# Kernel tuning notes

Hardware: AMD Instinct MI355X
Metric: run time of the kernel (lower is better)

The kernel has to match this reference:

```python
import jax, jax.numpy as jnp
import numpy as np

NUM_GRAPHS = 64  # number of graphs in the batch for global_mean_pool
BN_EPS = 1e-5


def setup_inputs() -> dict:
    key = jax.random.key(0)
    ks = jax.random.split(key, 8)
    N, E, D, H, O = 100000, 1600000, 128, 128, 32
    x = jax.random.normal(ks[0], (N, D), dtype=jnp.float32)
    edge_index = jax.random.randint(ks[1], (2, E), 0, N, dtype=jnp.int64)
    batch = jnp.sort(jax.random.randint(ks[2], (N,), 0, NUM_GRAPHS, dtype=jnp.int64))
    s = 1.0 / np.sqrt(D)
    W0 = (jax.random.normal(ks[3], (D, H), dtype=jnp.float32) * s)
    b0 = jnp.zeros((H,), jnp.float32)
    g0 = jnp.ones((H,), jnp.float32)
    be0 = jnp.zeros((H,), jnp.float32)
    W1 = (jax.random.normal(ks[4], (H, H), dtype=jnp.float32) * s)
    b1 = jnp.zeros((H,), jnp.float32)
    g1 = jnp.ones((H,), jnp.float32)
    be1 = jnp.zeros((H,), jnp.float32)
    Wfc = (jax.random.normal(ks[5], (H, O), dtype=jnp.float32) * s)
    bfc = jnp.zeros((O,), jnp.float32)
    return dict(x=x, edge_index=edge_index, batch=batch,
                W0=W0, b0=b0, g0=g0, be0=be0,
                W1=W1, b1=b1, g1=g1, be1=be1,
                Wfc=Wfc, bfc=bfc)


def reference(x, edge_index, batch, W0, b0, g0, be0, W1, b1, g1, be1, Wfc, bfc):
    N = x.shape[0]
    loops = jnp.arange(N, dtype=edge_index.dtype)
    src = jnp.concatenate([edge_index[0], loops])  # [E+N]
    dst = jnp.concatenate([edge_index[1], loops])
    # GCN symmetric normalization on A + I
    deg = jax.ops.segment_sum(jnp.ones_like(dst, jnp.float32), dst, num_segments=N)
    dinv = jnp.where(deg > 0, jax.lax.rsqrt(deg), 0.0)
    norm = dinv[src] * dinv[dst]  # [E+N]

    def gcn_layer(h, W, b):
        h = h @ W                                   # [N, H] transform first (PyG GCNConv)
        msg = h[src] * norm[:, None]                # gather + scale
        agg = jax.ops.segment_sum(msg, dst, num_segments=N)  # scatter-add
        return agg + b

    def bn_relu(h, g, be):  # BatchNorm1d (batch stats, biased var) + ReLU
        mu = h.mean(axis=0)
        var = h.var(axis=0)
        return jax.nn.relu((h - mu) * jax.lax.rsqrt(var + BN_EPS) * g + be)

    h = bn_relu(gcn_layer(x, W0, b0), g0, be0)
    h = bn_relu(gcn_layer(h, W1, b1), g1, be1)

    # global_mean_pool over graph assignment
    cnt = jax.ops.segment_sum(jnp.ones((N,), jnp.float32), batch, num_segments=NUM_GRAPHS)
    pooled = jax.ops.segment_sum(h, batch, num_segments=NUM_GRAPHS)
    pooled = pooled / jnp.maximum(cnt, 1.0)[:, None]
    return pooled @ Wfc + bfc  # [NUM_GRAPHS, out_dim]
```

## Files before the change

### kernel.cpp

```cpp
#include <hip/hip_runtime.h>

typedef short bf16x8 __attribute__((ext_vector_type(8)));
typedef float f32x4 __attribute__((ext_vector_type(4)));

#define NBLK 512
#define NSTAT 512

__device__ __forceinline__ unsigned short f2bf(float f) {
    unsigned u = __float_as_uint(f);
    u += 0x7fffu + ((u >> 16) & 1u);
    return (unsigned short)(u >> 16);
}
__device__ __forceinline__ float bflo(unsigned u) { return __uint_as_float(u << 16); }
__device__ __forceinline__ float bfhi(unsigned u) { return __uint_as_float(u & 0xffff0000u); }


__global__ __launch_bounds__(256) void kb_count(const int* __restrict__ dst, int E, int nb,
                                                int chunk, int* __restrict__ counts) {
    __shared__ int h[512];
    for (int i = threadIdx.x; i < 512; i += 256) h[i] = 0;
    __syncthreads();
    int e0 = blockIdx.x * chunk, e1 = min(e0 + chunk, E);
    for (int e = e0 + threadIdx.x; e < e1; e += 256) atomicAdd(&h[dst[e] >> 8], 1);
    __syncthreads();
    for (int b = threadIdx.x; b < nb; b += 256) counts[b * NBLK + blockIdx.x] = h[b];
}

__global__ __launch_bounds__(NBLK) void kb_offsets(int* __restrict__ counts,
                                                   int* __restrict__ total) {
    __shared__ int s[NBLK];
    int b = blockIdx.x, t = threadIdx.x;
    int v = counts[b * NBLK + t];
    s[t] = v; __syncthreads();
    for (int off = 1; off < NBLK; off <<= 1) {
        int x = (t >= off) ? s[t - off] : 0;
        __syncthreads();
        s[t] += x;
        __syncthreads();
    }
    counts[b * NBLK + t] = s[t] - v;
    if (t == NBLK - 1) total[b] = s[t];
}

__global__ __launch_bounds__(512) void kb_base(const int* __restrict__ total, int nb,
                                               int* __restrict__ bbase) {
    __shared__ int s[512];
    int t = threadIdx.x;
    int v = (t < nb) ? total[t] : 0;
    s[t] = v; __syncthreads();
    for (int off = 1; off < 512; off <<= 1) {
        int x = (t >= off) ? s[t - off] : 0;
        __syncthreads();
        s[t] += x;
        __syncthreads();
    }
    if (t < nb) bbase[t] = s[t] - v;
}

__global__ __launch_bounds__(NBLK) void kb_scatter(const int* __restrict__ src,
                                                   const int* __restrict__ dst, int E, int nb,
                                                   int chunk,
                                                   const int* __restrict__ counts,
                                                   const int* __restrict__ bbase,
                                                   int2* __restrict__ rec) {
    __shared__ int cur[512];
    int t = threadIdx.x;
    if (t < nb) cur[t] = bbase[t] + counts[t * NBLK + blockIdx.x];
    __syncthreads();
    int e0 = blockIdx.x * chunk, e1 = min(e0 + chunk, E);
    for (int e = e0 + t; e < e1; e += NBLK) {
        int s = src[e], d = dst[e];
        int pos = atomicAdd(&cur[d >> 8], 1);
        rec[pos] = make_int2(s, d);
    }
}

__global__ __launch_bounds__(256) void kb_deg(const int2* __restrict__ rec,
                                              const int* __restrict__ bbase,
                                              const int* __restrict__ total,
                                              int* __restrict__ deg,
                                              float* __restrict__ dinv, int N) {
    __shared__ int dc[256];
    int b = blockIdx.x, t = threadIdx.x;
    dc[t] = 0; __syncthreads();
    int r0 = bbase[b], r1 = r0 + total[b];
    for (int i = r0 + t; i < r1; i += 256) atomicAdd(&dc[rec[i].y & 255], 1);
    __syncthreads();
    int gn = b * 256 + t;
    if (gn < N) {
        int d = dc[t];
        deg[gn] = d;
        dinv[gn] = rsqrtf((float)(d + 1));
    }
}

__global__ __launch_bounds__(256) void k_scan_part(const int* __restrict__ deg, int N,
                                                   int* __restrict__ part) {
    int base = blockIdx.x * 1024 + threadIdx.x * 4;
    int s = 0;
#pragma unroll
    for (int i = 0; i < 4; ++i) {
        int idx = base + i;
        if (idx < N) s += (deg[idx] + 7) & ~7;
    }
    __shared__ int red[256];
    red[threadIdx.x] = s; __syncthreads();
    for (int off = 128; off > 0; off >>= 1) {
        if (threadIdx.x < off) red[threadIdx.x] += red[threadIdx.x + off];
        __syncthreads();
    }
    if (threadIdx.x == 0) part[blockIdx.x] = red[0];
}
__global__ void k_scan_mid(int* part, int nb) {
    if (threadIdx.x == 0 && blockIdx.x == 0) {
        int run = 0;
        for (int i = 0; i < nb; ++i) { int t = part[i]; part[i] = run; run += t; }
    }
}
__global__ __launch_bounds__(256) void k_scan_final(const int* __restrict__ deg, int N,
                                                    const int* __restrict__ part,
                                                    int* __restrict__ rowptr) {
    int t = threadIdx.x;
    int base = blockIdx.x * 1024 + t * 4;
    int v[4]; int s = 0;
#pragma unroll
    for (int i = 0; i < 4; ++i) {
        int idx = base + i;
        v[i] = (idx < N) ? ((deg[idx] + 7) & ~7) : 0;
        s += v[i];
    }
    __shared__ int sc[256];
    sc[t] = s; __syncthreads();
    for (int off = 1; off < 256; off <<= 1) {
        int x = (t >= off) ? sc[t - off] : 0;
        __syncthreads();
        sc[t] += x;
        __syncthreads();
    }
    int excl = sc[t] - s + part[blockIdx.x];
#pragma unroll
    for (int i = 0; i < 4; ++i) {
        int idx = base + i;
        if (idx < N) { rowptr[idx] = excl; excl += v[i]; }
    }
}

__global__ __launch_bounds__(256) void kb_place(const int2* __restrict__ rec,
                                                const int* __restrict__ bbase,
                                                const int* __restrict__ total,
                                                const int* __restrict__ rowptr,
                                                const float* __restrict__ dinv,
                                                int2* __restrict__ csr, int N) {
    __shared__ int cur[256];
    int b = blockIdx.x, t = threadIdx.x;
    int gn = b * 256 + t;
    int rp = (gn < N) ? rowptr[gn] : 0;
    cur[t] = rp;
    __syncthreads();
    int r0 = bbase[b], r1 = r0 + total[b];
    for (int i = r0 + t; i < r1; i += 256) {
        int2 rc = rec[i];
        int pos = atomicAdd(&cur[rc.y & 255], 1);
        float w = dinv[rc.x] * dinv[rc.y];
        csr[pos] = make_int2(rc.x, __float_as_int(w));
    }
    __syncthreads();
    if (gn < N) {
        int end = cur[t];
        int pe = rp + ((end - rp + 7) & ~7);
        for (int i = end; i < pe; ++i) csr[i] = make_int2(0, 0);
    }
}

__global__ __launch_bounds__(256) void k_wprep(const float* __restrict__ W0,
                                               const float* __restrict__ W1,
                                               unsigned short* __restrict__ W0t,
                                               unsigned short* __restrict__ W1t) {
    int tt = blockIdx.x * 256 + threadIdx.x;
    const float* W = (tt < 2048) ? W0 : W1;
    unsigned short* Wt = (tt < 2048) ? W0t : W1t;
    int t = tt & 2047;
    int f = t >> 6, lane = t & 63;
    int kc = f >> 3, nt = f & 7;
    int kbase = kc * 32 + (lane >> 4) * 8;
    int n = nt * 16 + (lane & 15);
    unsigned short t8[8];
#pragma unroll
    for (int j = 0; j < 8; ++j) t8[j] = f2bf(W[(size_t)(kbase + j) * 128 + n]);
    unsigned short* o = &Wt[(size_t)t * 8];
    *(ushort4*)&o[0] = *(ushort4*)&t8[0];
    *(ushort4*)&o[4] = *(ushort4*)&t8[4];
}

__global__ __launch_bounds__(256) void k_gemm(const void* __restrict__ Xv,
                                              const unsigned short* __restrict__ Wt,
                                              const float* __restrict__ scale,
                                              const float* __restrict__ shift,
                                              unsigned short* __restrict__ Hout,
                                              int N, int xbf16) {
    __shared__ unsigned short sX[64 * 136];
    const int tid = threadIdx.x;
    const int rowBase = blockIdx.x * 64;

    if (!xbf16) {
        const float* X = (const float*)Xv;
#pragma unroll
        for (int i = 0; i < 8; ++i) {
            int f4 = tid + 256 * i;
            int r = f4 >> 5; int k4 = (f4 & 31) * 4;
            int gr = rowBase + r;
            float4 v = make_float4(0.f, 0.f, 0.f, 0.f);
            if (gr < N) v = *(const float4*)&X[(size_t)gr * 128 + k4];
            ushort4 p;
            p.x = f2bf(v.x); p.y = f2bf(v.y); p.z = f2bf(v.z); p.w = f2bf(v.w);
            *(ushort4*)&sX[r * 136 + k4] = p;
        }
    } else {
        const int4* X = (const int4*)Xv;
#pragma unroll
        for (int i = 0; i < 4; ++i) {
            int f8 = tid + 256 * i;
            int r = f8 >> 4; int k8 = (f8 & 15) * 8;
            int gr = rowBase + r;
            int4 u = make_int4(0, 0, 0, 0);
            if (gr < N) u = X[(size_t)gr * 16 + (f8 & 15)];
            float fv[8] = { bflo(u.x), bfhi(u.x), bflo(u.y), bfhi(u.y),
                            bflo(u.z), bfhi(u.z), bflo(u.w), bfhi(u.w) };
            unsigned short t8[8];
#pragma unroll
            for (int j = 0; j < 8; ++j)
                t8[j] = f2bf(fmaxf(fmaf(fv[j], scale[k8 + j], shift[k8 + j]), 0.f));
            *(ushort4*)&sX[r * 136 + k8]     = *(ushort4*)&t8[0];
            *(ushort4*)&sX[r * 136 + k8 + 4] = *(ushort4*)&t8[4];
        }
    }
    __syncthreads();

    const int lane = tid & 63, wave = tid >> 6;
    const int m = lane & 15, q = lane >> 4;
    const int rowOff = (wave * 16 + m) * 136 + q * 8;
    f32x4 acc[8];
#pragma unroll
    for (int nt = 0; nt < 8; ++nt) acc[nt] = (f32x4){0.f, 0.f, 0.f, 0.f};
    const bf16x8* WtF = (const bf16x8*)Wt;
#pragma unroll
    for (int kc = 0; kc < 4; ++kc) {
        bf16x8 xb = *(const bf16x8*)&sX[rowOff + kc * 32];
#pragma unroll
        for (int nt = 0; nt < 8; ++nt) {
            bf16x8 wa = WtF[(kc * 8 + nt) * 64 + lane];
            acc[nt] = __builtin_amdgcn_mfma_f32_16x16x32_bf16(wa, xb, acc[nt], 0, 0, 0);
        }
    }
    int grow = rowBase + wave * 16 + m;
    if (grow < N) {
#pragma unroll
        for (int nt = 0; nt < 8; ++nt) {
            ushort4 p;
            p.x = f2bf(acc[nt][0]); p.y = f2bf(acc[nt][1]);
            p.z = f2bf(acc[nt][2]); p.w = f2bf(acc[nt][3]);
            *(ushort4*)&Hout[(size_t)grow * 128 + nt * 16 + q * 4] = p;
        }
    }
}

__global__ __launch_bounds__(256) void k_agg(const unsigned short* __restrict__ H,
                                             const int* __restrict__ rowptr,
                                             const int* __restrict__ deg,
                                             const int2* __restrict__ csr,
                                             const float* __restrict__ dinv,
                                             const float* __restrict__ bias,
                                             unsigned* __restrict__ out, int N) {
    int wave = threadIdx.x >> 6;
    int lane = threadIdx.x & 63;
    int node = blockIdx.x * 4 + wave;
    if (node >= N) return;
    const unsigned* Hu = (const unsigned*)H;
    int start = rowptr[node];
    int pd = (deg[node] + 7) & ~7;
    float a0 = 0.f, a1 = 0.f;
    const int4* cp = (const int4*)(csr + start);
    int j = 0;
    for (; j + 16 <= pd; j += 16) {
        int4 q0 = cp[0], q1 = cp[1], q2 = cp[2], q3 = cp[3];
        int4 q4 = cp[4], q5 = cp[5], q6 = cp[6], q7 = cp[7];
        cp += 8;
        unsigned u0 = Hu[(size_t)q0.x * 64 + lane];
        unsigned u1 = Hu[(size_t)q0.z * 64 + lane];
        unsigned u2 = Hu[(size_t)q1.x * 64 + lane];
        unsigned u3 = Hu[(size_t)q1.z * 64 + lane];
        unsigned u4 = Hu[(size_t)q2.x * 64 + lane];
        unsigned u5 = Hu[(size_t)q2.z * 64 + lane];
        unsigned u6 = Hu[(size_t)q3.x * 64 + lane];
        unsigned u7 = Hu[(size_t)q3.z * 64 + lane];
        unsigned u8 = Hu[(size_t)q4.x * 64 + lane];
        unsigned u9 = Hu[(size_t)q4.z * 64 + lane];
        unsigned uA = Hu[(size_t)q5.x * 64 + lane];
        unsigned uB = Hu[(size_t)q5.z * 64 + lane];
        unsigned uC = Hu[(size_t)q6.x * 64 + lane];
        unsigned uD = Hu[(size_t)q6.z * 64 + lane];
        unsigned uE = Hu[(size_t)q7.x * 64 + lane];
        unsigned uF = Hu[(size_t)q7.z * 64 + lane];
        float w0 = __int_as_float(q0.y), w1 = __int_as_float(q0.w);
        float w2 = __int_as_float(q1.y), w3 = __int_as_float(q1.w);
        float w4 = __int_as_float(q2.y), w5 = __int_as_float(q2.w);
        float w6 = __int_as_float(q3.y), w7 = __int_as_float(q3.w);
        float w8 = __int_as_float(q4.y), w9 = __int_as_float(q4.w);
        float wA = __int_as_float(q5.y), wB = __int_as_float(q5.w);
        float wC = __int_as_float(q6.y), wD = __int_as_float(q6.w);
        float wE = __int_as_float(q7.y), wF = __int_as_float(q7.w);
        a0 = fmaf(w0, bflo(u0), a0); a1 = fmaf(w0, bfhi(u0), a1);
        a0 = fmaf(w1, bflo(u1), a0); a1 = fmaf(w1, bfhi(u1), a1);
        a0 = fmaf(w2, bflo(u2), a0); a1 = fmaf(w2, bfhi(u2), a1);
        a0 = fmaf(w3, bflo(u3), a0); a1 = fmaf(w3, bfhi(u3), a1);
        a0 = fmaf(w4, bflo(u4), a0); a1 = fmaf(w4, bfhi(u4), a1);
        a0 = fmaf(w5, bflo(u5), a0); a1 = fmaf(w5, bfhi(u5), a1);
        a0 = fmaf(w6, bflo(u6), a0); a1 = fmaf(w6, bfhi(u6), a1);
        a0 = fmaf(w7, bflo(u7), a0); a1 = fmaf(w7, bfhi(u7), a1);
        a0 = fmaf(w8, bflo(u8), a0); a1 = fmaf(w8, bfhi(u8), a1);
        a0 = fmaf(w9, bflo(u9), a0); a1 = fmaf(w9, bfhi(u9), a1);
        a0 = fmaf(wA, bflo(uA), a0); a1 = fmaf(wA, bfhi(uA), a1);
        a0 = fmaf(wB, bflo(uB), a0); a1 = fmaf(wB, bfhi(uB), a1);
        a0 = fmaf(wC, bflo(uC), a0); a1 = fmaf(wC, bfhi(uC), a1);
        a0 = fmaf(wD, bflo(uD), a0); a1 = fmaf(wD, bfhi(uD), a1);
        a0 = fmaf(wE, bflo(uE), a0); a1 = fmaf(wE, bfhi(uE), a1);
        a0 = fmaf(wF, bflo(uF), a0); a1 = fmaf(wF, bfhi(uF), a1);
    }
    if (j < pd) {
        int4 q0 = cp[0], q1 = cp[1], q2 = cp[2], q3 = cp[3];
        unsigned u0 = Hu[(size_t)q0.x * 64 + lane];
        unsigned u1 = Hu[(size_t)q0.z * 64 + lane];
        unsigned u2 = Hu[(size_t)q1.x * 64 + lane];
        unsigned u3 = Hu[(size_t)q1.z * 64 + lane];
        unsigned u4 = Hu[(size_t)q2.x * 64 + lane];
        unsigned u5 = Hu[(size_t)q2.z * 64 + lane];
        unsigned u6 = Hu[(size_t)q3.x * 64 + lane];
        unsigned u7 = Hu[(size_t)q3.z * 64 + lane];
        float w0 = __int_as_float(q0.y), w1 = __int_as_float(q0.w);
        float w2 = __int_as_float(q1.y), w3 = __int_as_float(q1.w);
        float w4 = __int_as_float(q2.y), w5 = __int_as_float(q2.w);
        float w6 = __int_as_float(q3.y), w7 = __int_as_float(q3.w);
        a0 = fmaf(w0, bflo(u0), a0); a1 = fmaf(w0, bfhi(u0), a1);
        a0 = fmaf(w1, bflo(u1), a0); a1 = fmaf(w1, bfhi(u1), a1);
        a0 = fmaf(w2, bflo(u2), a0); a1 = fmaf(w2, bfhi(u2), a1);
        a0 = fmaf(w3, bflo(u3), a0); a1 = fmaf(w3, bfhi(u3), a1);
        a0 = fmaf(w4, bflo(u4), a0); a1 = fmaf(w4, bfhi(u4), a1);
        a0 = fmaf(w5, bflo(u5), a0); a1 = fmaf(w5, bfhi(u5), a1);
        a0 = fmaf(w6, bflo(u6), a0); a1 = fmaf(w6, bfhi(u6), a1);
        a0 = fmaf(w7, bflo(u7), a0); a1 = fmaf(w7, bfhi(u7), a1);
    }
    {
        float dn = dinv[node];
        float w = dn * dn;
        unsigned u = Hu[(size_t)node * 64 + lane];
        a0 = fmaf(w, bflo(u), a0);
        a1 = fmaf(w, bfhi(u), a1);
    }
    float2 bv = ((const float2*)bias)[lane];
    a0 += bv.x; a1 += bv.y;
    out[(size_t)node * 64 + lane] = (unsigned)f2bf(a0) | ((unsigned)f2bf(a1) << 16);
}

__global__ __launch_bounds__(256) void k_stats(const int4* __restrict__ B4, int N,
                                               float* __restrict__ P1,
                                               float* __restrict__ P2) {
    int tid = threadIdx.x;
    int lane = tid & 63, wave = tid >> 6;
    int c = lane & 15;
    int rsub = lane >> 4;
    float s1[8] = {0.f,0.f,0.f,0.f,0.f,0.f,0.f,0.f};
    float s2[8] = {0.f,0.f,0.f,0.f,0.f,0.f,0.f,0.f};
    for (int r = blockIdx.x * 16 + wave * 4 + rsub; r < N; r += NSTAT * 16) {
        int4 u = B4[(size_t)r * 16 + c];
        float f[8] = { bflo(u.x), bfhi(u.x), bflo(u.y), bfhi(u.y),
                       bflo(u.z), bfhi(u.z), bflo(u.w), bfhi(u.w) };
#pragma unroll
        for (int j = 0; j < 8; ++j) { s1[j] += f[j]; s2[j] = fmaf(f[j], f[j], s2[j]); }
    }
#pragma unroll
    for (int j = 0; j < 8; ++j) {
        s1[j] += __shfl_xor(s1[j], 16, 64);
        s1[j] += __shfl_xor(s1[j], 32, 64);
        s2[j] += __shfl_xor(s2[j], 16, 64);
        s2[j] += __shfl_xor(s2[j], 32, 64);
    }
    __shared__ float ls1[4][128], ls2[4][128];
    if (rsub == 0) {
#pragma unroll
        for (int j = 0; j < 8; ++j) { ls1[wave][c * 8 + j] = s1[j]; ls2[wave][c * 8 + j] = s2[j]; }
    }
    __syncthreads();
    if (tid < 128) {
        P1[blockIdx.x * 128 + tid] = ls1[0][tid] + ls1[1][tid] + ls1[2][tid] + ls1[3][tid];
        P2[blockIdx.x * 128 + tid] = ls2[0][tid] + ls2[1][tid] + ls2[2][tid] + ls2[3][tid];
    }
}

__global__ __launch_bounds__(256) void k_bnfinal(const float* __restrict__ P1,
                          const float* __restrict__ P2,
                          const float* __restrict__ g, const float* __restrict__ be,
                          float* __restrict__ scale, float* __restrict__ shift,
                          float invN) {
    __shared__ float sm[256];
    int t = threadIdx.x;
    int c = t & 127;
    const float* P = (t < 128) ? P1 : P2;
    float s = 0.f;
    for (int b = 0; b < NSTAT; ++b) s += P[b * 128 + c];
    sm[t] = s;
    __syncthreads();
    if (t < 128) {
        float mu = sm[t] * invN;
        float var = sm[t + 128] * invN - mu * mu;
        float sc = g[t] * rsqrtf(var + 1e-5f);
        scale[t] = sc;
        shift[t] = fmaf(-mu, sc, be[t]);
    }
}

__global__ __launch_bounds__(256) void k_hist(const int* __restrict__ batch, int N,
                                              int* __restrict__ gcnt) {
    __shared__ int h[64];
    if (threadIdx.x < 64) h[threadIdx.x] = 0;
    __syncthreads();
    for (int i = blockIdx.x * 256 + threadIdx.x; i < N; i += gridDim.x * 256)
        atomicAdd(&h[batch[i]], 1);
    __syncthreads();
    if (threadIdx.x < 64 && h[threadIdx.x]) atomicAdd(&gcnt[threadIdx.x], h[threadIdx.x]);
}

__global__ __launch_bounds__(256) void k_pool(const int4* __restrict__ B4,
                                              const float* __restrict__ scale,
                                              const float* __restrict__ shift,
                                              const int* __restrict__ batch, int N,
                                              int rpb, float* __restrict__ pooled) {
    int tid = threadIdx.x;
    int c = tid & 15;
    int rh = tid >> 4;
    int r0 = blockIdx.x * rpb;
    int r1 = min(r0 + rpb, N);
    float sc[8], sh[8];
#pragma unroll
    for (int j = 0; j < 8; ++j) { sc[j] = scale[c * 8 + j]; sh[j] = shift[c * 8 + j]; }
    float acc[8] = {0.f,0.f,0.f,0.f,0.f,0.f,0.f,0.f};
    int cur = -1;
    for (int r = r0 + rh; r < r1; r += 16) {
        int g = batch[r];
        if (g != cur) {
            if (cur >= 0) {
#pragma unroll
                for (int j = 0; j < 8; ++j)
                    atomicAdd(&pooled[cur * 128 + c * 8 + j], acc[j]);
            }
#pragma unroll
            for (int j = 0; j < 8; ++j) acc[j] = 0.f;
            cur = g;
        }
        int4 u = B4[(size_t)r * 16 + c];
        float f[8] = { bflo(u.x), bfhi(u.x), bflo(u.y), bfhi(u.y),
                       bflo(u.z), bfhi(u.z), bflo(u.w), bfhi(u.w) };
#pragma unroll
        for (int j = 0; j < 8; ++j) acc[j] += fmaxf(fmaf(f[j], sc[j], sh[j]), 0.f);
    }
    if (cur >= 0) {
#pragma unroll
        for (int j = 0; j < 8; ++j)
            atomicAdd(&pooled[cur * 128 + c * 8 + j], acc[j]);
    }
}

__global__ __launch_bounds__(256) void k_fc(const float* __restrict__ pooled,
                                            const int* __restrict__ gcnt,
                                            const float* __restrict__ Wfc,
                                            const float* __restrict__ bfc,
                                            float* __restrict__ out) {
    int idx = blockIdx.x * 256 + threadIdx.x;
    if (idx >= 64 * 32) return;
    int g = idx >> 5, o = idx & 31;
    float inv = 1.f / fmaxf((float)gcnt[g], 1.f);
    float acc = bfc[o];
    for (int k = 0; k < 128; ++k)
        acc = fmaf(pooled[g * 128 + k] * inv, Wfc[k * 32 + o], acc);
    out[idx] = acc;
}

extern "C" void kernel_launch(void* const* d_in, const int* in_sizes, int n_in,
                              void* d_out, int out_size, void* d_ws, size_t ws_size,
                              hipStream_t stream) {
    const float* x    = (const float*)d_in[0];
    const int*  eidx  = (const int*)d_in[1];
    const int*  batch = (const int*)d_in[2];
    const float* W0 = (const float*)d_in[3];
    const float* b0 = (const float*)d_in[4];
    const float* g0 = (const float*)d_in[5];
    const float* be0 = (const float*)d_in[6];
    const float* W1 = (const float*)d_in[7];
    const float* b1 = (const float*)d_in[8];
    const float* g1 = (const float*)d_in[9];
    const float* be1 = (const float*)d_in[10];
    const float* Wfc = (const float*)d_in[11];
    const float* bfc = (const float*)d_in[12];
    float* out = (float*)d_out;

    const int N = in_sizes[0] / 128;
    const int E = in_sizes[1] / 2;
    const int* esrc = eidx;
    const int* edst = eidx + E;
    const int NB = (N + 255) >> 8;
    const size_t paddedE = (size_t)E + 7 * (size_t)N;

    char* base = (char*)d_ws;
    size_t off = 0;
    auto take = [&](size_t bytes) -> char* {
        char* p = base + off;
        off = (off + bytes + 255) & ~(size_t)255;
        return p;
    };
    unsigned short* hA = (unsigned short*)take((size_t)N * 128 * 2);
    int2* rec = (int2*)hA;
    unsigned* B = (unsigned*)take((size_t)N * 64 * 4);
    int2* csr   = (int2*)take(paddedE * 8);
    int* rowptr = (int*)take((size_t)N * 4);
    int* deg    = (int*)take((size_t)N * 4);
    float* dinv = (float*)take((size_t)N * 4);
    int* counts = (int*)take((size_t)512 * NBLK * 4);
    int* total  = (int*)take(512 * 4);
    int* bbase  = (int*)take(512 * 4);
    int* part   = (int*)take(1024 * 4);
    unsigned short* W0t = (unsigned short*)take(16384 * 2);
    unsigned short* W1t = (unsigned short*)take(16384 * 2);
    float* P1 = (float*)take((size_t)NSTAT * 128 * 4);
    float* P2 = (float*)take((size_t)NSTAT * 128 * 4);
    char* zeroB0 = base + off;
    float* pooled = (float*)take(64 * 128 * 4);
    int*   gcnt   = (int*)take(64 * 4);
    size_t zeroB_bytes = (size_t)((base + off) - zeroB0);
    float* scale1 = (float*)take(128 * 4);
    float* shift1 = (float*)take(128 * 4);
    float* scale2 = (float*)take(128 * 4);
    float* shift2 = (float*)take(128 * 4);
    (void)ws_size; (void)n_in; (void)out_size;

    hipMemsetAsync(zeroB0, 0, zeroB_bytes, stream);

    k_wprep<<<16, 256, 0, stream>>>(W0, W1, W0t, W1t);

    const int CH256 = (E + NBLK - 1) / NBLK;
    kb_count<<<NBLK, 256, 0, stream>>>(edst, E, NB, CH256, counts);
    kb_offsets<<<NB, NBLK, 0, stream>>>(counts, total);
    kb_base<<<1, 512, 0, stream>>>(total, NB, bbase);
    kb_scatter<<<NBLK, NBLK, 0, stream>>>(esrc, edst, E, NB, CH256, counts, bbase, rec);
    kb_deg<<<NB, 256, 0, stream>>>(rec, bbase, total, deg, dinv, N);
    const int nbScan = (N + 1023) / 1024;
    k_scan_part<<<nbScan, 256, 0, stream>>>(deg, N, part);
    k_scan_mid<<<1, 64, 0, stream>>>(part, nbScan);
    k_scan_final<<<nbScan, 256, 0, stream>>>(deg, N, part, rowptr);
    kb_place<<<NB, 256, 0, stream>>>(rec, bbase, total, rowptr, dinv, csr, N);

    const int gGemm = (N + 63) / 64;
    const int gAgg  = (N + 3) / 4;
    const float invN = 1.0f / (float)N;

    k_gemm<<<gGemm, 256, 0, stream>>>(x, W0t, scale1, shift1, hA, N, 0);
    k_agg<<<gAgg, 256, 0, stream>>>(hA, rowptr, deg, csr, dinv, b0, B, N);
    k_stats<<<NSTAT, 256, 0, stream>>>((const int4*)B, N, P1, P2);
    k_bnfinal<<<1, 256, 0, stream>>>(P1, P2, g0, be0, scale1, shift1, invN);

    k_gemm<<<gGemm, 256, 0, stream>>>(B, W1t, scale1, shift1, hA, N, 1);
    k_agg<<<gAgg, 256, 0, stream>>>(hA, rowptr, deg, csr, dinv, b1, B, N);
    k_stats<<<NSTAT, 256, 0, stream>>>((const int4*)B, N, P1, P2);
    k_bnfinal<<<1, 256, 0, stream>>>(P1, P2, g1, be1, scale2, shift2, invN);

    k_hist<<<256, 256, 0, stream>>>(batch, N, gcnt);
    const int rpb = (N + 511) / 512;
    k_pool<<<(N + rpb - 1) / rpb, 256, 0, stream>>>((const int4*)B, scale2, shift2, batch, N, rpb, pooled);
    k_fc<<<8, 256, 0, stream>>>(pooled, gcnt, Wfc, bfc, out);
}
```

Baseline: 452.0 us.

## Fuse BN stats into aggregation, fold row-pointer scan into degree/place kernels

```diff
diff --git a/kernel.cpp b/kernel.cpp
--- a/kernel.cpp
+++ b/kernel.cpp
@@ -4,7 +4,6 @@
 typedef float f32x4 __attribute__((ext_vector_type(4)));
 
 #define NBLK 512
-#define NSTAT 512
 
 __device__ __forceinline__ unsigned short f2bf(float f) {
     unsigned u = __float_as_uint(f);
@@ -42,11 +41,11 @@
     if (t == NBLK - 1) total[b] = s[t];
 }
 
-__global__ __launch_bounds__(512) void kb_base(const int* __restrict__ total, int nb,
-                                               int* __restrict__ bbase) {
+__global__ __launch_bounds__(512) void kb_base(const int* __restrict__ in, int nb,
+                                               int* __restrict__ outb) {
     __shared__ int s[512];
     int t = threadIdx.x;
-    int v = (t < nb) ? total[t] : 0;
+    int v = (t < nb) ? in[t] : 0;
     s[t] = v; __syncthreads();
     for (int off = 1; off < 512; off <<= 1) {
         int x = (t >= off) ? s[t - off] : 0;
@@ -54,7 +53,7 @@
         s[t] += x;
         __syncthreads();
     }
-    if (t < nb) bbase[t] = s[t] - v;
+    if (t < nb) outb[t] = s[t] - v;
 }
 
 __global__ __launch_bounds__(NBLK) void kb_scatter(const int* __restrict__ src,
@@ -79,7 +78,8 @@
                                               const int* __restrict__ bbase,
                                               const int* __restrict__ total,
                                               int* __restrict__ deg,
-                                              float* __restrict__ dinv, int N) {
+                                              float* __restrict__ dinv,
+                                              int* __restrict__ padsum, int N) {
     __shared__ int dc[256];
     int b = blockIdx.x, t = threadIdx.x;
     dc[t] = 0; __syncthreads();
@@ -87,74 +87,44 @@
     for (int i = r0 + t; i < r1; i += 256) atomicAdd(&dc[rec[i].y & 255], 1);
     __syncthreads();
     int gn = b * 256 + t;
+    int d = dc[t];
+    int pd = (gn < N) ? ((d + 7) & ~7) : 0;
     if (gn < N) {
-        int d = dc[t];
         deg[gn] = d;
         dinv[gn] = rsqrtf((float)(d + 1));
     }
-}
-
-__global__ __launch_bounds__(256) void k_scan_part(const int* __restrict__ deg, int N,
-                                                   int* __restrict__ part) {
-    int base = blockIdx.x * 1024 + threadIdx.x * 4;
-    int s = 0;
-#pragma unroll
-    for (int i = 0; i < 4; ++i) {
-        int idx = base + i;
-        if (idx < N) s += (deg[idx] + 7) & ~7;
-    }
-    __shared__ int red[256];
-    red[threadIdx.x] = s; __syncthreads();
+    __syncthreads();
+    dc[t] = pd; __syncthreads();
     for (int off = 128; off > 0; off >>= 1) {
-        if (threadIdx.x < off) red[threadIdx.x] += red[threadIdx.x + off];
-        __syncthreads();
-    }
-    if (threadIdx.x == 0) part[blockIdx.x] = red[0];
-}
-__global__ void k_scan_mid(int* part, int nb) {
-    if (threadIdx.x == 0 && blockIdx.x == 0) {
-        int run = 0;
-        for (int i = 0; i < nb; ++i) { int t = part[i]; part[i] = run; run += t; }
-    }
-}
-__global__ __launch_bounds__(256) void k_scan_final(const int* __restrict__ deg, int N,
-                                                    const int* __restrict__ part,
-                                                    int* __restrict__ rowptr) {
-    int t = threadIdx.x;
-    int base = blockIdx.x * 1024 + t * 4;
-    int v[4]; int s = 0;
-#pragma unroll
-    for (int i = 0; i < 4; ++i) {
-        int idx = base + i;
-        v[i] = (idx < N) ? ((deg[idx] + 7) & ~7) : 0;
-        s += v[i];
-    }
-    __shared__ int sc[256];
-    sc[t] = s; __syncthreads();
-    for (int off = 1; off < 256; off <<= 1) {
-        int x = (t >= off) ? sc[t - off] : 0;
-        __syncthreads();
-        sc[t] += x;
-        __syncthreads();
-    }
-    int excl = sc[t] - s + part[blockIdx.x];
-#pragma unroll
-    for (int i = 0; i < 4; ++i) {
-        int idx = base + i;
-        if (idx < N) { rowptr[idx] = excl; excl += v[i]; }
-    }
+        if (t < off) dc[t] += dc[t + off];
+        __syncthreads();
+    }
+    if (t == 0) padsum[b] = dc[0];
 }
 
 __global__ __launch_bounds__(256) void kb_place(const int2* __restrict__ rec,
                                                 const int* __restrict__ bbase,
                                                 const int* __restrict__ total,
-                                                const int* __restrict__ rowptr,
+                                                const int* __restrict__ bucketBase,
+                                                const int* __restrict__ deg,
                                                 const float* __restrict__ dinv,
-                                                int2* __restrict__ csr, int N) {
+                                                int2* __restrict__ csr,
+                                                int* __restrict__ rowptr, int N) {
+    __shared__ int sc[256];
     __shared__ int cur[256];
     int b = blockIdx.x, t = threadIdx.x;
     int gn = b * 256 + t;
-    int rp = (gn < N) ? rowptr[gn] : 0;
+    int d = (gn < N) ? deg[gn] : 0;
+    int pd = (d + 7) & ~7;
+    sc[t] = pd; __syncthreads();
+    for (int off = 1; off < 256; off <<= 1) {
+        int x = (t >= off) ? sc[t - off] : 0;
+        __syncthreads();
+        sc[t] += x;
+        __syncthreads();
+    }
+    int rp = bucketBase[b] + sc[t] - pd;
+    if (gn < N) rowptr[gn] = rp;
     cur[t] = rp;
     __syncthreads();
     int r0 = bbase[b], r1 = r0 + total[b];
@@ -167,7 +137,7 @@
     __syncthreads();
     if (gn < N) {
         int end = cur[t];
-        int pe = rp + ((end - rp + 7) & ~7);
+        int pe = rp + pd;
         for (int i = end; i < pe; ++i) csr[i] = make_int2(0, 0);
     }
 }
@@ -175,8 +145,13 @@
 __global__ __launch_bounds__(256) void k_wprep(const float* __restrict__ W0,
                                                const float* __restrict__ W1,
                                                unsigned short* __restrict__ W0t,
-                                               unsigned short* __restrict__ W1t) {
+                                               unsigned short* __restrict__ W1t,
+                                               float* __restrict__ pooled,
+                                               int* __restrict__ gcnt) {
     int tt = blockIdx.x * 256 + threadIdx.x;
+    pooled[tt] = 0.f;
+    pooled[tt + 4096] = 0.f;
+    if (tt < 64) gcnt[tt] = 0;
     const float* W = (tt < 2048) ? W0 : W1;
     unsigned short* Wt = (tt < 2048) ? W0t : W1t;
     int t = tt & 2047;
@@ -270,129 +245,114 @@
                                              const int2* __restrict__ csr,
                                              const float* __restrict__ dinv,
                                              const float* __restrict__ bias,
-                                             unsigned* __restrict__ out, int N) {
-    int wave = threadIdx.x >> 6;
-    int lane = threadIdx.x & 63;
-    int node = blockIdx.x * 4 + wave;
-    if (node >= N) return;
+                                             unsigned* __restrict__ out,
+                                             float* __restrict__ P1,
+                                             float* __restrict__ P2, int N) {
+    int tid = threadIdx.x;
+    int wave = tid >> 6;
+    int lane = tid & 63;
     const unsigned* Hu = (const unsigned*)H;
-    int start = rowptr[node];
-    int pd = (deg[node] + 7) & ~7;
-    float a0 = 0.f, a1 = 0.f;
-    const int4* cp = (const int4*)(csr + start);
-    int j = 0;
-    for (; j + 16 <= pd; j += 16) {
-        int4 q0 = cp[0], q1 = cp[1], q2 = cp[2], q3 = cp[3];
-        int4 q4 = cp[4], q5 = cp[5], q6 = cp[6], q7 = cp[7];
-        cp += 8;
-        unsigned u0 = Hu[(size_t)q0.x * 64 + lane];
-        unsigned u1 = Hu[(size_t)q0.z * 64 + lane];
-        unsigned u2 = Hu[(size_t)q1.x * 64 + lane];
-        unsigned u3 = Hu[(size_t)q1.z * 64 + lane];
-        unsigned u4 = Hu[(size_t)q2.x * 64 + lane];
-        unsigned u5 = Hu[(size_t)q2.z * 64 + lane];
-        unsigned u6 = Hu[(size_t)q3.x * 64 + lane];
-        unsigned u7 = Hu[(size_t)q3.z * 64 + lane];
-        unsigned u8 = Hu[(size_t)q4.x * 64 + lane];
-        unsigned u9 = Hu[(size_t)q4.z * 64 + lane];
-        unsigned uA = Hu[(size_t)q5.x * 64 + lane];
-        unsigned uB = Hu[(size_t)q5.z * 64 + lane];
-        unsigned uC = Hu[(size_t)q6.x * 64 + lane];
-        unsigned uD = Hu[(size_t)q6.z * 64 + lane];
-        unsigned uE = Hu[(size_t)q7.x * 64 + lane];
-        unsigned uF = Hu[(size_t)q7.z * 64 + lane];
-        float w0 = __int_as_float(q0.y), w1 = __int_as_float(q0.w);
-        float w2 = __int_as_float(q1.y), w3 = __int_as_float(q1.w);
-        float w4 = __int_as_float(q2.y), w5 = __int_as_float(q2.w);
-        float w6 = __int_as_float(q3.y), w7 = __int_as_float(q3.w);
-        float w8 = __int_as_float(q4.y), w9 = __int_as_float(q4.w);
-        float wA = __int_as_float(q5.y), wB = __int_as_float(q5.w);
-        float wC = __int_as_float(q6.y), wD = __int_as_float(q6.w);
-        float wE = __int_as_float(q7.y), wF = __int_as_float(q7.w);
-        a0 = fmaf(w0, bflo(u0), a0); a1 = fmaf(w0, bfhi(u0), a1);
-        a0 = fmaf(w1, bflo(u1), a0); a1 = fmaf(w1, bfhi(u1), a1);
-        a0 = fmaf(w2, bflo(u2), a0); a1 = fmaf(w2, bfhi(u2), a1);
-        a0 = fmaf(w3, bflo(u3), a0); a1 = fmaf(w3, bfhi(u3), a1);
-        a0 = fmaf(w4, bflo(u4), a0); a1 = fmaf(w4, bfhi(u4), a1);
-        a0 = fmaf(w5, bflo(u5), a0); a1 = fmaf(w5, bfhi(u5), a1);
-        a0 = fmaf(w6, bflo(u6), a0); a1 = fmaf(w6, bfhi(u6), a1);
-        a0 = fmaf(w7, bflo(u7), a0); a1 = fmaf(w7, bfhi(u7), a1);
-        a0 = fmaf(w8, bflo(u8), a0); a1 = fmaf(w8, bfhi(u8), a1);
-        a0 = fmaf(w9, bflo(u9), a0); a1 = fmaf(w9, bfhi(u9), a1);
-        a0 = fmaf(wA, bflo(uA), a0); a1 = fmaf(wA, bfhi(uA), a1);
-        a0 = fmaf(wB, bflo(uB), a0); a1 = fmaf(wB, bfhi(uB), a1);
-        a0 = fmaf(wC, bflo(uC), a0); a1 = fmaf(wC, bfhi(uC), a1);
-        a0 = fmaf(wD, bflo(uD), a0); a1 = fmaf(wD, bfhi(uD), a1);
-        a0 = fmaf(wE, bflo(uE), a0); a1 = fmaf(wE, bfhi(uE), a1);
-        a0 = fmaf(wF, bflo(uF), a0); a1 = fmaf(wF, bfhi(uF), a1);
-    }
-    if (j < pd) {
-        int4 q0 = cp[0], q1 = cp[1], q2 = cp[2], q3 = cp[3];
-        unsigned u0 = Hu[(size_t)q0.x * 64 + lane];
-        unsigned u1 = Hu[(size_t)q0.z * 64 + lane];
-        unsigned u2 = Hu[(size_t)q1.x * 64 + lane];
-        unsigned u3 = Hu[(size_t)q1.z * 64 + lane];
-        unsigned u4 = Hu[(size_t)q2.x * 64 + lane];
-        unsigned u5 = Hu[(size_t)q2.z * 64 + lane];
-        unsigned u6 = Hu[(size_t)q3.x * 64 + lane];
-        unsigned u7 = Hu[(size_t)q3.z * 64 + lane];
-        float w0 = __int_as_float(q0.y), w1 = __int_as_float(q0.w);
-        float w2 = __int_as_float(q1.y), w3 = __int_as_float(q1.w);
-        float w4 = __int_as_float(q2.y), w5 = __int_as_float(q2.w);
-        float w6 = __int_as_float(q3.y), w7 = __int_as_float(q3.w);
-        a0 = fmaf(w0, bflo(u0), a0); a1 = fmaf(w0, bfhi(u0), a1);
-        a0 = fmaf(w1, bflo(u1), a0); a1 = fmaf(w1, bfhi(u1), a1);
-        a0 = fmaf(w2, bflo(u2), a0); a1 = fmaf(w2, bfhi(u2), a1);
-        a0 = fmaf(w3, bflo(u3), a0); a1 = fmaf(w3, bfhi(u3), a1);
-        a0 = fmaf(w4, bflo(u4), a0); a1 = fmaf(w4, bfhi(u4), a1);
-        a0 = fmaf(w5, bflo(u5), a0); a1 = fmaf(w5, bfhi(u5), a1);
-        a0 = fmaf(w6, bflo(u6), a0); a1 = fmaf(w6, bfhi(u6), a1);
-        a0 = fmaf(w7, bflo(u7), a0); a1 = fmaf(w7, bfhi(u7), a1);
-    }
-    {
-        float dn = dinv[node];
-        float w = dn * dn;
-        unsigned u = Hu[(size_t)node * 64 + lane];
-        a0 = fmaf(w, bflo(u), a0);
-        a1 = fmaf(w, bfhi(u), a1);
-    }
     float2 bv = ((const float2*)bias)[lane];
-    a0 += bv.x; a1 += bv.y;
-    out[(size_t)node * 64 + lane] = (unsigned)f2bf(a0) | ((unsigned)f2bf(a1) << 16);
-}
-
-__global__ __launch_bounds__(256) void k_stats(const int4* __restrict__ B4, int N,
-                                               float* __restrict__ P1,
-                                               float* __restrict__ P2) {
-    int tid = threadIdx.x;
-    int lane = tid & 63, wave = tid >> 6;
-    int c = lane & 15;
-    int rsub = lane >> 4;
-    float s1[8] = {0.f,0.f,0.f,0.f,0.f,0.f,0.f,0.f};
-    float s2[8] = {0.f,0.f,0.f,0.f,0.f,0.f,0.f,0.f};
-    for (int r = blockIdx.x * 16 + wave * 4 + rsub; r < N; r += NSTAT * 16) {
-        int4 u = B4[(size_t)r * 16 + c];
-        float f[8] = { bflo(u.x), bfhi(u.x), bflo(u.y), bfhi(u.y),
-                       bflo(u.z), bfhi(u.z), bflo(u.w), bfhi(u.w) };
-#pragma unroll
-        for (int j = 0; j < 8; ++j) { s1[j] += f[j]; s2[j] = fmaf(f[j], f[j], s2[j]); }
-    }
-#pragma unroll
-    for (int j = 0; j < 8; ++j) {
-        s1[j] += __shfl_xor(s1[j], 16, 64);
-        s1[j] += __shfl_xor(s1[j], 32, 64);
-        s2[j] += __shfl_xor(s2[j], 16, 64);
-        s2[j] += __shfl_xor(s2[j], 32, 64);
+    float s1a = 0.f, s1b = 0.f, s2a = 0.f, s2b = 0.f;
+    int nodeBase = blockIdx.x * 64 + wave * 16;
+    int nEnd = min(nodeBase + 16, N);
+#pragma unroll 1
+    for (int node = nodeBase; node < nEnd; ++node) {
+        int start = rowptr[node];
+        int pd = (deg[node] + 7) & ~7;
+        float a0 = 0.f, a1 = 0.f;
+        const int4* cp = (const int4*)(csr + start);
+        int j = 0;
+#pragma unroll 1
+        for (; j + 16 <= pd; j += 16) {
+            int4 q0 = cp[0], q1 = cp[1], q2 = cp[2], q3 = cp[3];
+            int4 q4 = cp[4], q5 = cp[5], q6 = cp[6], q7 = cp[7];
+            cp += 8;
+            unsigned u0 = Hu[(size_t)q0.x * 64 + lane];
+            unsigned u1 = Hu[(size_t)q0.z * 64 + lane];
+            unsigned u2 = Hu[(size_t)q1.x * 64 + lane];
+            unsigned u3 = Hu[(size_t)q1.z * 64 + lane];
+            unsigned u4 = Hu[(size_t)q2.x * 64 + lane];
+            unsigned u5 = Hu[(size_t)q2.z * 64 + lane];
+            unsigned u6 = Hu[(size_t)q3.x * 64 + lane];
+            unsigned u7 = Hu[(size_t)q3.z * 64 + lane];
+            unsigned u8 = Hu[(size_t)q4.x * 64 + lane];
+            unsigned u9 = Hu[(size_t)q4.z * 64 + lane];
+            unsigned uA = Hu[(size_t)q5.x * 64 + lane];
+            unsigned uB = Hu[(size_t)q5.z * 64 + lane];
+            unsigned uC = Hu[(size_t)q6.x * 64 + lane];
+            unsigned uD = Hu[(size_t)q6.z * 64 + lane];
+            unsigned uE = Hu[(size_t)q7.x * 64 + lane];
+            unsigned uF = Hu[(size_t)q7.z * 64 + lane];
+            float w0 = __int_as_float(q0.y), w1 = __int_as_float(q0.w);
+            float w2 = __int_as_float(q1.y), w3 = __int_as_float(q1.w);
+            float w4 = __int_as_float(q2.y), w5 = __int_as_float(q2.w);
+            float w6 = __int_as_float(q3.y), w7 = __int_as_float(q3.w);
+            float w8 = __int_as_float(q4.y), w9 = __int_as_float(q4.w);
+            float wA = __int_as_float(q5.y), wB = __int_as_float(q5.w);
+            float wC = __int_as_float(q6.y), wD = __int_as_float(q6.w);
+            float wE = __int_as_float(q7.y), wF = __int_as_float(q7.w);
+            a0 = fmaf(w0, bflo(u0), a0); a1 = fmaf(w0, bfhi(u0), a1);
+            a0 = fmaf(w1, bflo(u1), a0); a1 = fmaf(w1, bfhi(u1), a1);
+            a0 = fmaf(w2, bflo(u2), a0); a1 = fmaf(w2, bfhi(u2), a1);
+            a0 = fmaf(w3, bflo(u3), a0); a1 = fmaf(w3, bfhi(u3), a1);
+            a0 = fmaf(w4, bflo(u4), a0); a1 = fmaf(w4, bfhi(u4), a1);
+            a0 = fmaf(w5, bflo(u5), a0); a1 = fmaf(w5, bfhi(u5), a1);
+            a0 = fmaf(w6, bflo(u6), a0); a1 = fmaf(w6, bfhi(u6), a1);
+            a0 = fmaf(w7, bflo(u7), a0); a1 = fmaf(w7, bfhi(u7), a1);
+            a0 = fmaf(w8, bflo(u8), a0); a1 = fmaf(w8, bfhi(u8), a1);
+            a0 = fmaf(w9, bflo(u9), a0); a1 = fmaf(w9, bfhi(u9), a1);
+            a0 = fmaf(wA, bflo(uA), a0); a1 = fmaf(wA, bfhi(uA), a1);
+            a0 = fmaf(wB, bflo(uB), a0); a1 = fmaf(wB, bfhi(uB), a1);
+            a0 = fmaf(wC, bflo(uC), a0); a1 = fmaf(wC, bfhi(uC), a1);
+            a0 = fmaf(wD, bflo(uD), a0); a1 = fmaf(wD, bfhi(uD), a1);
+            a0 = fmaf(wE, bflo(uE), a0); a1 = fmaf(wE, bfhi(uE), a1);
+            a0 = fmaf(wF, bflo(uF), a0); a1 = fmaf(wF, bfhi(uF), a1);
+        }
+        if (j < pd) {
+            int4 q0 = cp[0], q1 = cp[1], q2 = cp[2], q3 = cp[3];
+            unsigned u0 = Hu[(size_t)q0.x * 64 + lane];
+            unsigned u1 = Hu[(size_t)q0.z * 64 + lane];
+            unsigned u2 = Hu[(size_t)q1.x * 64 + lane];
+            unsigned u3 = Hu[(size_t)q1.z * 64 + lane];
+            unsigned u4 = Hu[(size_t)q2.x * 64 + lane];
+            unsigned u5 = Hu[(size_t)q2.z * 64 + lane];
+            unsigned u6 = Hu[(size_t)q3.x * 64 + lane];
+            unsigned u7 = Hu[(size_t)q3.z * 64 + lane];
+            float w0 = __int_as_float(q0.y), w1 = __int_as_float(q0.w);
+            float w2 = __int_as_float(q1.y), w3 = __int_as_float(q1.w);
+            float w4 = __int_as_float(q2.y), w5 = __int_as_float(q2.w);
+            float w6 = __int_as_float(q3.y), w7 = __int_as_float(q3.w);
+            a0 = fmaf(w0, bflo(u0), a0); a1 = fmaf(w0, bfhi(u0), a1);
+            a0 = fmaf(w1, bflo(u1), a0); a1 = fmaf(w1, bfhi(u1), a1);
+            a0 = fmaf(w2, bflo(u2), a0); a1 = fmaf(w2, bfhi(u2), a1);
+            a0 = fmaf(w3, bflo(u3), a0); a1 = fmaf(w3, bfhi(u3), a1);
+            a0 = fmaf(w4, bflo(u4), a0); a1 = fmaf(w4, bfhi(u4), a1);
+            a0 = fmaf(w5, bflo(u5), a0); a1 = fmaf(w5, bfhi(u5), a1);
+            a0 = fmaf(w6, bflo(u6), a0); a1 = fmaf(w6, bfhi(u6), a1);
+            a0 = fmaf(w7, bflo(u7), a0); a1 = fmaf(w7, bfhi(u7), a1);
+        }
+        {
+            float dn = dinv[node];
+            float w = dn * dn;
+            unsigned u = Hu[(size_t)node * 64 + lane];
+            a0 = fmaf(w, bflo(u), a0);
+            a1 = fmaf(w, bfhi(u), a1);
+        }
+        a0 += bv.x; a1 += bv.y;
+        out[(size_t)node * 64 + lane] = (unsigned)f2bf(a0) | ((unsigned)f2bf(a1) << 16);
+        s1a += a0; s2a = fmaf(a0, a0, s2a);
+        s1b += a1; s2b = fmaf(a1, a1, s2b);
     }
     __shared__ float ls1[4][128], ls2[4][128];
-    if (rsub == 0) {
-#pragma unroll
-        for (int j = 0; j < 8; ++j) { ls1[wave][c * 8 + j] = s1[j]; ls2[wave][c * 8 + j] = s2[j]; }
-    }
+    ls1[wave][2 * lane]     = s1a;
+    ls1[wave][2 * lane + 1] = s1b;
+    ls2[wave][2 * lane]     = s2a;
+    ls2[wave][2 * lane + 1] = s2b;
     __syncthreads();
     if (tid < 128) {
-        P1[blockIdx.x * 128 + tid] = ls1[0][tid] + ls1[1][tid] + ls1[2][tid] + ls1[3][tid];
-        P2[blockIdx.x * 128 + tid] = ls2[0][tid] + ls2[1][tid] + ls2[2][tid] + ls2[3][tid];
+        P1[(size_t)blockIdx.x * 128 + tid] = ls1[0][tid] + ls1[1][tid] + ls1[2][tid] + ls1[3][tid];
+        P2[(size_t)blockIdx.x * 128 + tid] = ls2[0][tid] + ls2[1][tid] + ls2[2][tid] + ls2[3][tid];
     }
 }
 
@@ -400,40 +360,35 @@
                           const float* __restrict__ P2,
                           const float* __restrict__ g, const float* __restrict__ be,
                           float* __restrict__ scale, float* __restrict__ shift,
-                          float invN) {
-    __shared__ float sm[256];
-    int t = threadIdx.x;
-    int c = t & 127;
-    const float* P = (t < 128) ? P1 : P2;
-    float s = 0.f;
-    for (int b = 0; b < NSTAT; ++b) s += P[b * 128 + c];
-    sm[t] = s;
-    __syncthreads();
-    if (t < 128) {
-        float mu = sm[t] * invN;
-        float var = sm[t + 128] * invN - mu * mu;
-        float sc = g[t] * rsqrtf(var + 1e-5f);
-        scale[t] = sc;
-        shift[t] = fmaf(-mu, sc, be[t]);
-    }
-}
-
-__global__ __launch_bounds__(256) void k_hist(const int* __restrict__ batch, int N,
-                                              int* __restrict__ gcnt) {
-    __shared__ int h[64];
-    if (threadIdx.x < 64) h[threadIdx.x] = 0;
-    __syncthreads();
-    for (int i = blockIdx.x * 256 + threadIdx.x; i < N; i += gridDim.x * 256)
-        atomicAdd(&h[batch[i]], 1);
-    __syncthreads();
-    if (threadIdx.x < 64 && h[threadIdx.x]) atomicAdd(&gcnt[threadIdx.x], h[threadIdx.x]);
+                          float invN, int nPart) {
+    int f = blockIdx.x, t = threadIdx.x;
+    float s1 = 0.f, s2 = 0.f;
+    for (int i = t; i < nPart; i += 256) {
+        s1 += P1[(size_t)i * 128 + f];
+        s2 += P2[(size_t)i * 128 + f];
+    }
+    __shared__ float l1[256], l2[256];
+    l1[t] = s1; l2[t] = s2;
+    __syncthreads();
+    for (int off = 128; off > 0; off >>= 1) {
+        if (t < off) { l1[t] += l1[t + off]; l2[t] += l2[t + off]; }
+        __syncthreads();
+    }
+    if (t == 0) {
+        float mu = l1[0] * invN;
+        float var = l2[0] * invN - mu * mu;
+        float sc = g[f] * rsqrtf(var + 1e-5f);
+        scale[f] = sc;
+        shift[f] = fmaf(-mu, sc, be[f]);
+    }
 }
 
 __global__ __launch_bounds__(256) void k_pool(const int4* __restrict__ B4,
                                               const float* __restrict__ scale,
                                               const float* __restrict__ shift,
                                               const int* __restrict__ batch, int N,
-                                              int rpb, float* __restrict__ pooled) {
+                                              int rpb, float* __restrict__ pooled,
+                                              int* __restrict__ gcnt) {
     int tid = threadIdx.x;
     int c = tid & 15;
     int rh = tid >> 4;
@@ -443,6 +398,7 @@
 #pragma unroll
     for (int j = 0; j < 8; ++j) { sc[j] = scale[c * 8 + j]; sh[j] = shift[c * 8 + j]; }
     float acc[8] = {0.f,0.f,0.f,0.f,0.f,0.f,0.f,0.f};
+    int cnt = 0;
     int cur = -1;
     for (int r = r0 + rh; r < r1; r += 16) {
         int g = batch[r];
@@ -451,9 +407,11 @@
 #pragma unroll
                 for (int j = 0; j < 8; ++j)
                     atomicAdd(&pooled[cur * 128 + c * 8 + j], acc[j]);
+                if (c == 0) atomicAdd(&gcnt[cur], cnt);
             }
 #pragma unroll
             for (int j = 0; j < 8; ++j) acc[j] = 0.f;
+            cnt = 0;
             cur = g;
         }
         int4 u = B4[(size_t)r * 16 + c];
@@ -461,11 +419,13 @@
                        bflo(u.z), bfhi(u.z), bflo(u.w), bfhi(u.w) };
 #pragma unroll
         for (int j = 0; j < 8; ++j) acc[j] += fmaxf(fmaf(f[j], sc[j], sh[j]), 0.f);
+        ++cnt;
     }
     if (cur >= 0) {
 #pragma unroll
         for (int j = 0; j < 8; ++j)
             atomicAdd(&pooled[cur * 128 + c * 8 + j], acc[j]);
+        if (c == 0) atomicAdd(&gcnt[cur], cnt);
     }
 }
 
@@ -508,6 +468,7 @@
     const int* edst = eidx + E;
     const int NB = (N + 255) >> 8;
     const size_t paddedE = (size_t)E + 7 * (size_t)N;
+    const int nPart = (N + 63) / 64;
 
     char* base = (char*)d_ws;
     size_t off = 0;
@@ -526,53 +487,43 @@
     int* counts = (int*)take((size_t)512 * NBLK * 4);
     int* total  = (int*)take(512 * 4);
     int* bbase  = (int*)take(512 * 4);
-    int* part   = (int*)take(1024 * 4);
+    int* padsum = (int*)take(512 * 4);
+    int* bucketBase = (int*)take(512 * 4);
     unsigned short* W0t = (unsigned short*)take(16384 * 2);
     unsigned short* W1t = (unsigned short*)take(16384 * 2);
-    float* P1 = (float*)take((size_t)NSTAT * 128 * 4);
-    float* P2 = (float*)take((size_t)NSTAT * 128 * 4);
-    char* zeroB0 = base + off;
+    float* P1 = (float*)take((size_t)nPart * 128 * 4);
+    float* P2 = (float*)take((size_t)nPart * 128 * 4);
     float* pooled = (float*)take(64 * 128 * 4);
     int*   gcnt   = (int*)take(64 * 4);
-    size_t zeroB_bytes = (size_t)((base + off) - zeroB0);
     float* scale1 = (float*)take(128 * 4);
     float* shift1 = (float*)take(128 * 4);
     float* scale2 = (float*)take(128 * 4);
     float* shift2 = (float*)take(128 * 4);
     (void)ws_size; (void)n_in; (void)out_size;
 
-    hipMemsetAsync(zeroB0, 0, zeroB_bytes, stream);
-
-    k_wprep<<<16, 256, 0, stream>>>(W0, W1, W0t, W1t);
+    k_wprep<<<16, 256, 0, stream>>>(W0, W1, W0t, W1t, pooled, gcnt);
 
     const int CH256 = (E + NBLK - 1) / NBLK;
     kb_count<<<NBLK, 256, 0, stream>>>(edst, E, NB, CH256, counts);
     kb_offsets<<<NB, NBLK, 0, stream>>>(counts, total);
     kb_base<<<1, 512, 0, stream>>>(total, NB, bbase);
     kb_scatter<<<NBLK, NBLK, 0, stream>>>(esrc, edst, E, NB, CH256, counts, bbase, rec);
-    kb_deg<<<NB, 256, 0, stream>>>(rec, bbase, total, deg, dinv, N);
-    const int nbScan = (N + 1023) / 1024;
-    k_scan_part<<<nbScan, 256, 0, stream>>>(deg, N, part);
-    k_scan_mid<<<1, 64, 0, stream>>>(part, nbScan);
-    k_scan_final<<<nbScan, 256, 0, stream>>>(deg, N, part, rowptr);
-    kb_place<<<NB, 256, 0, stream>>>(rec, bbase, total, rowptr, dinv, csr, N);
+    kb_deg<<<NB, 256, 0, stream>>>(rec, bbase, total, deg, dinv, padsum, N);
+    kb_base<<<1, 512, 0, stream>>>(padsum, NB, bucketBase);
+    kb_place<<<NB, 256, 0, stream>>>(rec, bbase, total, bucketBase, deg, dinv, csr, rowptr, N);
 
     const int gGemm = (N + 63) / 64;
-    const int gAgg  = (N + 3) / 4;
     const float invN = 1.0f / (float)N;
 
     k_gemm<<<gGemm, 256, 0, stream>>>(x, W0t, scale1, shift1, hA, N, 0);
-    k_agg<<<gAgg, 256, 0, stream>>>(hA, rowptr, deg, csr, dinv, b0, B, N);
-    k_stats<<<NSTAT, 256, 0, stream>>>((const int4*)B, N, P1, P2);
-    k_bnfinal<<<1, 256, 0, stream>>>(P1, P2, g0, be0, scale1, shift1, invN);
+    k_agg<<<nPart, 256, 0, stream>>>(hA, rowptr, deg, csr, dinv, b0, B, P1, P2, N);
+    k_bnfinal<<<128, 256, 0, stream>>>(P1, P2, g0, be0, scale1, shift1, invN, nPart);
 
     k_gemm<<<gGemm, 256, 0, stream>>>(B, W1t, scale1, shift1, hA, N, 1);
-    k_agg<<<gAgg, 256, 0, stream>>>(hA, rowptr, deg, csr, dinv, b1, B, N);
-    k_stats<<<NSTAT, 256, 0, stream>>>((const int4*)B, N, P1, P2);
-    k_bnfinal<<<1, 256, 0, stream>>>(P1, P2, g1, be1, scale2, shift2, invN);
-
-    k_hist<<<256, 256, 0, stream>>>(batch, N, gcnt);
+    k_agg<<<nPart, 256, 0, stream>>>(hA, rowptr, deg, csr, dinv, b1, B, P1, P2, N);
+    k_bnfinal<<<128, 256, 0, stream>>>(P1, P2, g1, be1, scale2, shift2, invN, nPart);
+
     const int rpb = (N + 511) / 512;
-    k_pool<<<(N + rpb - 1) / rpb, 256, 0, stream>>>((const int4*)B, scale2, shift2, batch, N, rpb, pooled);
+    k_pool<<<(N + rpb - 1) / rpb, 256, 0, stream>>>((const int4*)B, scale2, shift2, batch, N, rpb, pooled, gcnt);
     k_fc<<<8, 256, 0, stream>>>(pooled, gcnt, Wfc, bfc, out);
 }
```

After: 472.3 us. 1.04x slower.
